# Kernel optimization log

Hardware: AMD Instinct MI355X
Metric: run time of the kernel (lower is better)

## Reference

```python
import jax, jax.numpy as jnp
import numpy as np

N_NODE = 50000
EMB = 128
LAYERS = 2
B = 1024
L = 50
E = 1_600_000


def setup_inputs() -> dict:
    key = jax.random.key(0)
    ks = jax.random.split(key, 21)
    d = EMB
    stdv = 1.0 / np.sqrt(d)
    u = lambda k, shape: jax.random.uniform(k, shape, minval=-stdv, maxval=stdv, dtype=jnp.float32)
    inp = {
        'adj_row': jax.random.randint(ks[0], (E,), 0, N_NODE, dtype=jnp.int32),
        'adj_col': jax.random.randint(ks[1], (E,), 0, N_NODE, dtype=jnp.int32),
        'adj_val': jax.random.uniform(ks[2], (E,), dtype=jnp.float32) / 32.0,  # ~row-normalized sparse adjacency
        'embedding': jax.random.normal(ks[3], (N_NODE, d), dtype=jnp.float32) * 0.1,
        'session_item': jax.random.randint(ks[4], (B, L), 0, N_NODE, dtype=jnp.int32),  # 0 hits the zero pad row
        'session_len': jnp.full((B, 1), float(L), dtype=jnp.float32),
        'D': jax.random.uniform(ks[5], (B, B), dtype=jnp.float32) / B,
        'A_sess': jax.random.uniform(ks[6], (B, B), dtype=jnp.float32) / B,
        'A_gnn': jax.random.uniform(ks[7], (B, L, 2 * L), dtype=jnp.float32) / L,
        'alias_pos': jax.random.randint(ks[8], (B, L), 0, L, dtype=jnp.int32),
        'hidden': jax.random.normal(ks[9], (B, L, d), dtype=jnp.float32) * 0.1,
        'W_in': u(ks[10], (d, d)), 'b_in': u(ks[11], (d,)),
        'W_out': u(ks[12], (d, d)), 'b_out': u(ks[13], (d,)),
        'w_ih': u(ks[14], (3 * d, 2 * d)), 'b_ih': u(ks[15], (3 * d,)),
        'w_hh': u(ks[16], (3 * d, d)), 'b_hh': u(ks[17], (3 * d,)),
        'b_iah': u(ks[18], (d,)), 'b_oah': u(ks[19], (d,)),
    }
    return inp


def reference(adj_row, adj_col, adj_val, embedding, session_item, session_len,
              D, A_sess, A_gnn, alias_pos, hidden,
              W_in, b_in, W_out, b_out, w_ih, b_ih, w_hh, b_hh, b_iah, b_oah):
    # ---- HyperConv: layers of sparse (COO) adjacency @ embedding, summed over hops ----
    emb = embedding
    final = embedding
    for _ in range(LAYERS):
        emb = jax.ops.segment_sum(adj_val[:, None] * emb[adj_col], adj_row, num_segments=N_NODE)
        final = final + emb
    item_emb = final  # [N_NODE, d]

    # ---- LineConv: zero-padded gather + mean pool over session, then session-graph propagation ----
    pad_table = jnp.concatenate([jnp.zeros((1, EMB), embedding.dtype), embedding], axis=0)
    seq_h = pad_table[session_item]                      # [B, L, d]
    sess = jnp.sum(seq_h, axis=1) / session_len          # [B, d]
    DA = D @ A_sess                                      # [B, B]
    acc = sess
    s = sess
    for _ in range(LAYERS):
        s = DA @ s
        acc = acc + s
    session_emb = acc                                    # [B, d]

    # ---- GNN: gather per-session in/out adjacency rows, gated GRU-style update ----
    in_out = jnp.take_along_axis(A_gnn, alias_pos[:, :, None], axis=1)  # [B, L, 2L]
    h_in = hidden @ W_in.T + b_in
    h_out = hidden @ W_out.T + b_out
    input_in = jnp.einsum('bij,bjd->bid', in_out[:, :, :L], h_in) + b_iah
    input_out = jnp.einsum('bij,bjd->bid', in_out[:, :, L:], h_out) + b_oah
    inputs = jnp.concatenate([input_in, input_out], axis=2)             # [B, L, 2d]
    gi = inputs @ w_ih.T + b_ih
    gh = hidden @ w_hh.T + b_hh
    i_r, i_i, i_n = jnp.split(gi, 3, axis=2)
    h_r, h_i, h_n = jnp.split(gh, 3, axis=2)
    resetgate = jax.nn.sigmoid(i_r + h_r)
    inputgate = jax.nn.sigmoid(i_i + h_i)
    newgate = jnp.tanh(i_n + resetgate * h_n)
    hy = newgate + inputgate * (hidden - newgate)        # [B, L, d]

    return item_emb, session_emb, hy
```

## Files before the change

### kernel.cpp

```cpp
#include <hip/hip_runtime.h>

#define EMB 128
#define NN 50000
#define BB 1024
#define LL 50
#define NBK 49
#define NEB 512
#define NCONV 2048

typedef float f32x4 __attribute__((ext_vector_type(4)));
typedef float f32x2 __attribute__((ext_vector_type(2)));
typedef unsigned short u16;
typedef unsigned int u32;
typedef unsigned long long u64;
typedef u16 u16x4 __attribute__((ext_vector_type(4)));
typedef u32 u32x4 __attribute__((ext_vector_type(4)));
typedef short bf16x8 __attribute__((ext_vector_type(8)));

__device__ __forceinline__ float u2f(u16 u) {
    union { unsigned int i; float f; } v; v.i = ((unsigned int)u) << 16; return v.f;
}
__device__ __forceinline__ u16 f2b(float f) {
    union { float f; unsigned int i; } v; v.f = f;
    unsigned int i = v.i;
    return (u16)((i + 0x7FFFu + ((i >> 16) & 1u)) >> 16);
}
__device__ __forceinline__ float lo2f(u32 w) { return u2f((u16)(w & 0xffffu)); }
__device__ __forceinline__ float hi2f(u32 w) { return u2f((u16)(w >> 16)); }
__device__ __forceinline__ float sigmoidf_(float x) { return 1.f / (1.f + __expf(-x)); }
__device__ __forceinline__ float tanhf_(float x) {
    float e = __expf(-2.f * x);
    return (1.f - e) / (1.f + e);
}

__global__ __launch_bounds__(256) void prep_kernel(
    const float* __restrict__ emb, const float* __restrict__ A, const float* __restrict__ D,
    const float* __restrict__ whh,
    u16* __restrict__ emb_bf, u16* __restrict__ A_bf, u16* __restrict__ D_bf,
    u16* __restrict__ whh_bf,
    const int* __restrict__ rowi, int* __restrict__ bcnt,
    const float* __restrict__ w_ih, const float* __restrict__ W_in, const float* __restrict__ W_out,
    const float* __restrict__ b_in, const float* __restrict__ b_out,
    const float* __restrict__ b_iah, const float* __restrict__ b_oah, const float* __restrict__ b_ih,
    const float* __restrict__ b_hh,
    u16* __restrict__ WcT_bf, float* __restrict__ uf,
    int E, int chunk)
{
    __shared__ int lc[NBK];
    __shared__ float wrow[256];
    __shared__ float red[3][256];
    int tid = threadIdx.x;

    if (blockIdx.x >= NCONV) {
        int d = blockIdx.x - NCONV;
        int c = tid;
        wrow[c] = w_ih[d * 256 + c];
        __syncthreads();
        const float* W = (c < 128) ? W_in : W_out;
        const float* wr = wrow + ((c < 128) ? 0 : 128);
        int cc = c & 127;
        float acc = 0.f;
#pragma unroll 4
        for (int j = 0; j < 128; j++) acc += wr[j] * W[j * 128 + cc];
        WcT_bf[d * 256 + c] = f2b(acc);
        float p1 = (c < 128) ? b_in[c] * wrow[c] : 0.f;
        float p2 = (c >= 128) ? b_out[cc] * wrow[c] : 0.f;
        float p3 = (c < 128) ? b_iah[c] * wrow[c] : b_oah[cc] * wrow[c];
        red[0][c] = p1; red[1][c] = p2; red[2][c] = p3;
        __syncthreads();
        for (int off = 128; off > 0; off >>= 1) {
            if (c < off) {
                red[0][c] += red[0][c + off];
                red[1][c] += red[1][c + off];
                red[2][c] += red[2][c + off];
            }
            __syncthreads();
        }
        if (c == 0) {
            int g = d >> 7, dd = d & 127;
            float u1v = red[0][0];
            float u2v = red[1][0];
            float u3v = red[2][0] + b_ih[d];
            uf[dd * 12 + g] = u1v;
            uf[dd * 12 + 3 + g] = u2v;
            if (g == 0)      uf[dd * 12 + 6] = u3v + b_hh[dd];
            else if (g == 1) uf[dd * 12 + 7] = u3v + b_hh[128 + dd];
            else {
                uf[dd * 12 + 8]  = u3v;
                uf[dd * 12 + 9]  = b_hh[256 + dd];
                uf[dd * 12 + 10] = 0.f;
                uf[dd * 12 + 11] = 0.f;
            }
        }
        return;
    }

    int gid = blockIdx.x * 256 + tid;
    int stride = NCONV * 256;
    if (blockIdx.x < NEB) {
        if (tid < NBK) lc[tid] = 0;
        __syncthreads();
        int beg = blockIdx.x * chunk, end = min(E, beg + chunk);
        for (int e = beg + tid; e < end; e += 256)
            atomicAdd(&lc[rowi[e] >> 10], 1);
        __syncthreads();
        if (tid < NBK) bcnt[blockIdx.x * NBK + tid] = lc[tid];
    }
    for (int i = gid; i < 1600000; i += stride) {
        f32x4 v = *(const f32x4*)(emb + (size_t)i * 4);
        u16x4 p;
#pragma unroll
        for (int t = 0; t < 4; t++) p[t] = f2b(v[t]);
        *(u16x4*)(emb_bf + (size_t)i * 4) = p;
    }
    for (int i = gid; i < 2146304; i += stride) {
        const float* s; u16* d; int off;
        if (i < 1048576)      { s = A;   d = A_bf;   off = i; }
        else if (i < 2097152) { s = D;   d = D_bf;   off = i - 1048576; }
        else                  { s = whh; d = whh_bf; off = i - 2097152; }
        d[off] = f2b(s[off]);
    }
}

__global__ __launch_bounds__(512) void bktscan_kernel(
    const int* __restrict__ bcnt, int* __restrict__ sofs, int* __restrict__ btot)
{
    __shared__ int ps[512];
    int k = blockIdx.x, t = threadIdx.x;
    int c = bcnt[t * NBK + k];
    ps[t] = c; __syncthreads();
    for (int off = 1; off < 512; off <<= 1) {
        int v = (t >= off) ? ps[t - off] : 0;
        __syncthreads();
        ps[t] += v; __syncthreads();
    }
    sofs[t * NBK + k] = ps[t] - c;
    if (t == 511) btot[k] = ps[511];
}

__global__ __launch_bounds__(64) void btotal_kernel(
    const int* __restrict__ btot, int* __restrict__ bofs, int E)
{
    if (threadIdx.x == 0) {
        int run = 0;
        for (int k = 0; k < NBK; k++) { bofs[k] = run; run += btot[k]; }
        bofs[NBK] = E;
    }
}

__global__ __launch_bounds__(256) void emit_kernel(
    const int* __restrict__ rowi, const int* __restrict__ coli, const float* __restrict__ val,
    const int* __restrict__ sofs, const int* __restrict__ bofs,
    u64* __restrict__ egs, int E, int chunk)
{
    __shared__ int cur[NBK];
    int b = blockIdx.x, tid = threadIdx.x;
    if (tid < NBK) cur[tid] = bofs[tid] + sofs[b * NBK + tid];
    __syncthreads();
    int beg = b * chunk, end = min(E, beg + chunk);
    for (int e = beg + tid; e < end; e += 256) {
        int r = rowi[e];
        int slot = atomicAdd(&cur[r >> 10], 1);
        u64 entry = ((u64)(u32)(r & 1023) << 32)
                  | (u64)((u32)(u16)coli[e] | ((u32)f2b(val[e]) << 16));
        egs[slot] = entry;
    }
}

__global__ __launch_bounds__(1024) void binsort2_kernel(
    const u64* __restrict__ egs, const int* __restrict__ bofs,
    int* __restrict__ row_ptr, u32* __restrict__ eg, int E)
{
    __shared__ int cnt_s[1024];
    __shared__ int ps[1024];
    int k = blockIdx.x, tid = threadIdx.x;
    int r0 = k << 10;
    int beg = bofs[k], end = bofs[k + 1];
    cnt_s[tid] = 0;
    __syncthreads();
    for (int i = beg + tid; i < end; i += 1024)
        atomicAdd(&cnt_s[(int)(egs[i] >> 32)], 1);
    __syncthreads();
    int v = cnt_s[tid];
    ps[tid] = v; __syncthreads();
    for (int off = 1; off < 1024; off <<= 1) {
        int t = (tid >= off) ? ps[tid - off] : 0;
        __syncthreads();
        ps[tid] += t; __syncthreads();
    }
    int ex = beg + ps[tid] - v;
    if (r0 + tid <= NN) row_ptr[r0 + tid] = ex;
    if (k == NBK - 1 && tid == 1023) row_ptr[NN] = E;
    cnt_s[tid] = ex;
    __syncthreads();
    for (int i = beg + tid; i < end; i += 1024) {
        u64 entry = egs[i];
        int rlo = (int)(entry >> 32);
        int p = atomicAdd(&cnt_s[rlo], 1);
        eg[p] = (u32)entry;
    }
}

template<int FUSE>
__global__ __launch_bounds__(256) void gatherb_kernel(
    const int* __restrict__ row_ptr, const u32* __restrict__ eg,
    const u16* __restrict__ src, const float* __restrict__ emb0,
    u16* __restrict__ dst_bf, float* __restrict__ dst_f)
{
    int wave = threadIdx.x >> 6;
    int lane = threadIdx.x & 63;
    int g  = lane >> 4;
    int fl = lane & 15;
    int r = blockIdx.x * 4 + wave;
    if (r >= NN) return;
    int beg = row_ptr[r], end = row_ptr[r + 1];

    float acc[8];
#pragma unroll
    for (int t = 0; t < 8; t++) acc[t] = 0.f;

    if (beg < end) {
        int last = end - 1;
        int npair = (end - beg + 7) >> 3;
        u32 pkA = eg[min(beg + g, last)];
        u32 pkB = eg[min(beg + 4 + g, last)];
        float vA = (beg + g     < end) ? u2f((u16)(pkA >> 16)) : 0.f;
        float vB = (beg + 4 + g < end) ? u2f((u16)(pkB >> 16)) : 0.f;
        u32x4 xA = *(const u32x4*)(src + ((pkA & 0xffffu) << 7) + (fl << 3));
        u32x4 xB = *(const u32x4*)(src + ((pkB & 0xffffu) << 7) + (fl << 3));
        pkA = eg[min(beg + 8  + g, last)];
        pkB = eg[min(beg + 12 + g, last)];

        int e = beg;
        for (int p = 0; p < npair; p++) {
            float cvA = vA, cvB = vB;
            u32x4 cxA = xA, cxB = xB;
            int eN = e + 8;
            vA = (eN + g     < end) ? u2f((u16)(pkA >> 16)) : 0.f;
            vB = (eN + 4 + g < end) ? u2f((u16)(pkB >> 16)) : 0.f;
            xA = *(const u32x4*)(src + ((pkA & 0xffffu) << 7) + (fl << 3));
            xB = *(const u32x4*)(src + ((pkB & 0xffffu) << 7) + (fl << 3));
            int eS = e + 16;
            pkA = eg[min(eS + g, last)];
            pkB = eg[min(eS + 4 + g, last)];
#pragma unroll
            for (int t = 0; t < 4; t++) {
                acc[2 * t]     += cvA * lo2f(cxA[t]);
                acc[2 * t + 1] += cvA * hi2f(cxA[t]);
            }
#pragma unroll
            for (int t = 0; t < 4; t++) {
                acc[2 * t]     += cvB * lo2f(cxB[t]);
                acc[2 * t + 1] += cvB * hi2f(cxB[t]);
            }
            e += 8;
        }
    }

#pragma unroll
    for (int t = 0; t < 8; t++) {
        acc[t] += __shfl_xor(acc[t], 16);
        acc[t] += __shfl_xor(acc[t], 32);
    }

    if (lane < 16) {
        if (FUSE) {
            u32x4 s = *(const u32x4*)(src + ((u32)r << 7) + (lane << 3));
            const float* e0p = emb0 + ((size_t)r << 7) + (lane << 3);
            f32x4 e0a = *(const f32x4*)e0p;
            f32x4 e0b = *(const f32x4*)(e0p + 4);
            f32x4 o0, o1;
#pragma unroll
            for (int t = 0; t < 2; t++) {
                o0[2 * t]     = acc[2 * t]     + e0a[2 * t]     + lo2f(s[t]);
                o0[2 * t + 1] = acc[2 * t + 1] + e0a[2 * t + 1] + hi2f(s[t]);
                o1[2 * t]     = acc[4 + 2 * t]     + e0b[2 * t]     + lo2f(s[2 + t]);
                o1[2 * t + 1] = acc[4 + 2 * t + 1] + e0b[2 * t + 1] + hi2f(s[2 + t]);
            }
            float* dp = dst_f + ((size_t)r << 7) + (lane << 3);
            *(f32x4*)dp = o0;
            *(f32x4*)(dp + 4) = o1;
        } else {
            u32x4 w;
#pragma unroll
            for (int t = 0; t < 4; t++)
                w[t] = (u32)f2b(acc[2 * t]) | ((u32)f2b(acc[2 * t + 1]) << 16);
            *(u32x4*)(dst_bf + ((size_t)r << 7) + (lane << 3)) = w;
        }
    }
}

__global__ __launch_bounds__(128) void sess_pool_kernel(
    const int* __restrict__ items, const float* __restrict__ emb,
    const float* __restrict__ slen, float* __restrict__ sess, u16* __restrict__ sessT)
{
    int b = blockIdx.x, d = threadIdx.x;
    const int* it = items + b * LL;
    float acc = 0.f;
    for (int l = 0; l < LL; l++) {
        int idx = it[l];
        if (idx > 0) acc += emb[(size_t)(idx - 1) * EMB + d];
    }
    float v = acc / slen[b];
    sess[b * EMB + d] = v;
    sessT[d * BB + b] = f2b(v);
}

template<int WT, int WF, int FADD>
__global__ __launch_bounds__(256) void mm_mfma_kernel(
    const u16* __restrict__ M_bf, const u16* __restrict__ Xt_bf,
    u16* __restrict__ Ct_bf, float* __restrict__ C_f,
    const float* __restrict__ add1, const float* __restrict__ add2)
{
    int tid = threadIdx.x;
    int wv = tid >> 6, lane = tid & 63, cl = lane & 15, kg = lane >> 4;
    int rbase = blockIdx.x * 16;
    f32x4 acc[2];
    acc[0] = (f32x4)0.f; acc[1] = (f32x4)0.f;
    const u16* arow = M_bf + (size_t)(rbase + cl) * BB + kg * 8;
    const u16* brow = Xt_bf + (size_t)(wv * 32 + cl) * BB + kg * 8;
#pragma unroll 4
    for (int k0 = 0; k0 < BB; k0 += 32) {
        bf16x8 a  = *(const bf16x8*)(arow + k0);
        bf16x8 b0 = *(const bf16x8*)(brow + k0);
        bf16x8 b1 = *(const bf16x8*)(brow + (size_t)16 * BB + k0);
        acc[0] = __builtin_amdgcn_mfma_f32_16x16x32_bf16(a, b0, acc[0], 0, 0, 0);
        acc[1] = __builtin_amdgcn_mfma_f32_16x16x32_bf16(a, b1, acc[1], 0, 0, 0);
    }
#pragma unroll
    for (int nt = 0; nt < 2; nt++) {
        int col = (wv * 2 + nt) * 16 + cl;
#pragma unroll
        for (int j = 0; j < 4; j++) {
            int row = rbase + kg * 4 + j;
            size_t ix = (size_t)row * EMB + col;
            if (WF) {
                float v = acc[nt][j];
                if (FADD) v += add1[ix] + add2[ix];
                C_f[ix] = v;
            }
            if (WT) Ct_bf[(size_t)col * BB + row] = f2b(acc[nt][j]);
        }
    }
}

__global__ __launch_bounds__(512) void gnn_tail_kernel(
    const float* __restrict__ hidden,
    const float* __restrict__ A_gnn, const int* __restrict__ alias_pos,
    const u16* __restrict__ WcT_bf, const u16* __restrict__ w_hh_bf,
    const float* __restrict__ uf,
    float* __restrict__ hy)
{
    __shared__ __attribute__((aligned(16))) u16 smem[25600];
    u16* Hs  = smem;
    u16* As  = smem + 8192;
    u16* HsT = smem + 16384;
    u16* M2s = smem + 8192;
    __shared__ float rcs[64][2];

    int b = blockIdx.x;
    int tid = threadIdx.x;
    int wv = tid >> 6, lane = tid & 63, cl = lane & 15, kg = lane >> 4;

    int pr_row[4], pr_c4[4], ppos[4];
#pragma unroll
    for (int it = 0; it < 4; it++) {
        int i = tid + it * 512;
        pr_row[it] = i >> 5; pr_c4[it] = i & 31;
        ppos[it] = (pr_row[it] < LL) ? alias_pos[b * LL + pr_row[it]] : 0;
    }
    float av[4][4];
#pragma unroll
    for (int it = 0; it < 4; it++) {
        const float* ar = A_gnn + ((size_t)b * LL + ppos[it]) * (2 * LL);
#pragma unroll
        for (int t = 0; t < 4; t++) {
            int jp = pr_c4[it] * 4 + t;
            int col = (jp < 64) ? jp : (50 + (jp - 64));
            int ok = (pr_row[it] < LL) && ((jp < 64) ? (jp < LL) : ((jp - 64) < LL));
            av[it][t] = ok ? ar[col] : 0.f;
        }
    }
    const float* hsrc = hidden + (size_t)b * LL * EMB;
#pragma unroll
    for (int it = 0; it < 4; it++) {
        u16x4 p;
#pragma unroll
        for (int t = 0; t < 4; t++) p[t] = f2b(av[it][t]);
        *(u16x4*)((char*)As + pr_row[it] * 256 + ((pr_c4[it] * 8) ^ ((pr_row[it] & 7) << 4))) = p;
    }
#pragma unroll
    for (int i2 = 0; i2 < 4; i2++) {
        int lin = i2 * 512 + tid;
        int hrow = lin >> 5, hc4 = lin & 31;
        f32x4 v = (hrow < LL) ? *(const f32x4*)(hsrc + hrow * 128 + hc4 * 4) : (f32x4)0.f;
        u16x4 q;
#pragma unroll
        for (int t = 0; t < 4; t++) q[t] = f2b(v[t]);
        *(u16x4*)((char*)Hs + hrow * 256 + ((hc4 * 8) ^ ((hrow & 7) << 4))) = q;
    }
#pragma unroll
    for (int i2 = 0; i2 < 4; i2++) {
        int idx = i2 * 512 + tid;
        int c = idx & 127, rg = idx >> 7;
        int r0 = rg * 4;
        u16x4 p = (u16x4)0;
#pragma unroll
        for (int k = 0; k < 4; k++) {
            int row = r0 + k;
            p[k] = (row < LL) ? f2b(hsrc[row * 128 + c]) : (u16)0;
        }
        *(u16x4*)&HsT[c * 72 + r0] = p;
    }
    __syncthreads();

    if (tid < 128) {
        int row = tid >> 1, hf = tid & 1;
        float s = 0.f;
#pragma unroll
        for (int c4 = 0; c4 < 16; c4++) {
            u16x4 v = *(const u16x4*)((const char*)As + row * 256 +
                        ((hf * 128 + c4 * 8) ^ ((row & 7) << 4)));
            s += u2f(v[0]) + u2f(v[1]) + u2f(v[2]) + u2f(v[3]);
        }
        rcs[row][hf] = s;
    }

    {
        int h = wv >> 2, ct = wv & 3;
        f32x4 m2acc[4][2];
#pragma unroll
        for (int mt = 0; mt < 4; mt++) { m2acc[mt][0] = (f32x4)0.f; m2acc[mt][1] = (f32x4)0.f; }
#pragma unroll
        for (int ks = 0; ks < 2; ks++) {
            bf16x8 bb[2];
#pragma unroll
            for (int nt = 0; nt < 2; nt++) {
                int c = ct * 32 + nt * 16 + cl;
                bb[nt] = *(const bf16x8*)&HsT[c * 72 + ks * 32 + kg * 8];
            }
#pragma unroll
            for (int mt = 0; mt < 4; mt++) {
                int mr = mt * 16 + cl;
                bf16x8 aa = *(const bf16x8*)((const char*)As + mr * 256 +
                             ((h * 128 + ks * 64 + kg * 16) ^ ((mr & 7) << 4)));
#pragma unroll
                for (int nt = 0; nt < 2; nt++)
                    m2acc[mt][nt] = __builtin_amdgcn_mfma_f32_16x16x32_bf16(aa, bb[nt], m2acc[mt][nt], 0, 0, 0);
            }
        }
        __syncthreads();
#pragma unroll
        for (int mt = 0; mt < 4; mt++)
#pragma unroll
            for (int nt = 0; nt < 2; nt++) {
                int kcol = h * 128 + ct * 32 + nt * 16 + cl;
#pragma unroll
                for (int j = 0; j < 4; j++) {
                    int row = mt * 16 + kg * 4 + j;
                    *(u16*)((char*)M2s + row * 512 + ((kcol * 2) ^ ((row & 7) << 4))) =
                        f2b(m2acc[mt][nt][j]);
                }
            }
    }
    __syncthreads();

    int dl = wv * 16 + cl;
    f32x4 accR[4], accI[4], accN1[4], accN2[4];
#pragma unroll
    for (int mt = 0; mt < 4; mt++) {
        accR[mt] = (f32x4)0.f; accI[mt] = (f32x4)0.f;
        accN1[mt] = (f32x4)0.f; accN2[mt] = (f32x4)0.f;
    }

#pragma unroll
    for (int ks = 0; ks < 8; ks++) {
        {
            bf16x8 bw = *(const bf16x8*)(WcT_bf + (size_t)dl * 256 + ks * 32 + kg * 8);
#pragma unroll
            for (int mt = 0; mt < 4; mt++) {
                int mr = mt * 16 + cl;
                bf16x8 a = *(const bf16x8*)((const char*)M2s + mr * 512 +
                             ((ks * 64 + kg * 16) ^ ((mr & 7) << 4)));
                accR[mt] = __builtin_amdgcn_mfma_f32_16x16x32_bf16(a, bw, accR[mt], 0, 0, 0);
            }
        }
        {
            bf16x8 bw = *(const bf16x8*)(WcT_bf + (size_t)(128 + dl) * 256 + ks * 32 + kg * 8);
#pragma unroll
            for (int mt = 0; mt < 4; mt++) {
                int mr = mt * 16 + cl;
                bf16x8 a = *(const bf16x8*)((const char*)M2s + mr * 512 +
                             ((ks * 64 + kg * 16) ^ ((mr & 7) << 4)));
                accI[mt] = __builtin_amdgcn_mfma_f32_16x16x32_bf16(a, bw, accI[mt], 0, 0, 0);
            }
        }
        {
            bf16x8 bw = *(const bf16x8*)(WcT_bf + (size_t)(256 + dl) * 256 + ks * 32 + kg * 8);
#pragma unroll
            for (int mt = 0; mt < 4; mt++) {
                int mr = mt * 16 + cl;
                bf16x8 a = *(const bf16x8*)((const char*)M2s + mr * 512 +
                             ((ks * 64 + kg * 16) ^ ((mr & 7) << 4)));
                accN1[mt] = __builtin_amdgcn_mfma_f32_16x16x32_bf16(a, bw, accN1[mt], 0, 0, 0);
            }
        }
    }
#pragma unroll
    for (int ks = 0; ks < 4; ks++) {
        {
            bf16x8 bw = *(const bf16x8*)(w_hh_bf + (size_t)dl * 128 + ks * 32 + kg * 8);
#pragma unroll
            for (int mt = 0; mt < 4; mt++) {
                int mr = mt * 16 + cl;
                bf16x8 a = *(const bf16x8*)((const char*)Hs + mr * 256 +
                             ((ks * 64 + kg * 16) ^ ((mr & 7) << 4)));
                accR[mt] = __builtin_amdgcn_mfma_f32_16x16x32_bf16(a, bw, accR[mt], 0, 0, 0);
            }
        }
        {
            bf16x8 bw = *(const bf16x8*)(w_hh_bf + (size_t)(128 + dl) * 128 + ks * 32 + kg * 8);
#pragma unroll
            for (int mt = 0; mt < 4; mt++) {
                int mr = mt * 16 + cl;
                bf16x8 a = *(const bf16x8*)((const char*)Hs + mr * 256 +
                             ((ks * 64 + kg * 16) ^ ((mr & 7) << 4)));
                accI[mt] = __builtin_amdgcn_mfma_f32_16x16x32_bf16(a, bw, accI[mt], 0, 0, 0);
            }
        }
        {
            bf16x8 bw = *(const bf16x8*)(w_hh_bf + (size_t)(256 + dl) * 128 + ks * 32 + kg * 8);
#pragma unroll
            for (int mt = 0; mt < 4; mt++) {
                int mr = mt * 16 + cl;
                bf16x8 a = *(const bf16x8*)((const char*)Hs + mr * 256 +
                             ((ks * 64 + kg * 16) ^ ((mr & 7) << 4)));
                accN2[mt] = __builtin_amdgcn_mfma_f32_16x16x32_bf16(a, bw, accN2[mt], 0, 0, 0);
            }
        }
    }

    __builtin_amdgcn_sched_barrier(0);
    {
        const f32x4* ufp = (const f32x4*)(uf + dl * 12);
        f32x4 U0 = ufp[0];
        f32x4 U1 = ufp[1];
        f32x4 U2 = ufp[2];
        float* hyb = hy + (size_t)b * LL * 128 + dl;
#pragma unroll
        for (int mt = 0; mt < 4; mt++)
#pragma unroll
            for (int j = 0; j < 4; j++) {
                int row = mt * 16 + kg * 4 + j;
                if (row >= LL) continue;
                float cr = rcs[row][0], dr = rcs[row][1];
                float pr  = accR[mt][j]  + cr * U0[0] + dr * U0[3] + U1[2];
                float pi  = accI[mt][j]  + cr * U0[1] + dr * U1[0] + U1[3];
                float pn1 = accN1[mt][j] + cr * U0[2] + dr * U1[1] + U2[0];
                float pn2 = accN2[mt][j] + U2[1];
                float rg = sigmoidf_(pr);
                float ig = sigmoidf_(pi);
                float ng = tanhf_(pn1 + rg * pn2);
                u16 hb = *(const u16*)((const char*)Hs + row * 256 + ((dl * 2) ^ ((row & 7) << 4)));
                float h = u2f(hb);
                hyb[row * 128] = ng + ig * (h - ng);
            }
    }
}

extern "C" void kernel_launch(void* const* d_in, const int* in_sizes, int n_in,
                              void* d_out, int out_size, void* d_ws, size_t ws_size,
                              hipStream_t stream) {
    (void)n_in; (void)out_size; (void)ws_size;
    const int*   adj_row      = (const int*)d_in[0];
    const int*   adj_col      = (const int*)d_in[1];
    const float* adj_val      = (const float*)d_in[2];
    const float* embedding    = (const float*)d_in[3];
    const int*   session_item = (const int*)d_in[4];
    const float* session_len  = (const float*)d_in[5];
    const float* Dm           = (const float*)d_in[6];
    const float* A_sess       = (const float*)d_in[7];
    const float* A_gnn        = (const float*)d_in[8];
    const int*   alias_pos    = (const int*)d_in[9];
    const float* hidden       = (const float*)d_in[10];
    const float* W_in         = (const float*)d_in[11];
    const float* b_in         = (const float*)d_in[12];
    const float* W_out        = (const float*)d_in[13];
    const float* b_out        = (const float*)d_in[14];
    const float* w_ih         = (const float*)d_in[15];
    const float* b_ih         = (const float*)d_in[16];
    const float* w_hh         = (const float*)d_in[17];
    const float* b_hh         = (const float*)d_in[18];
    const float* b_iah        = (const float*)d_in[19];
    const float* b_oah        = (const float*)d_in[20];
    const int E = in_sizes[0];

    float* out0 = (float*)d_out;
    float* out1 = out0 + 6400000;
    float* out2 = out1 + 131072;

    float* ws = (float*)d_ws;
    u16*  emb_bf  = (u16*)ws;
    int*  bcnt  = (int*)(ws + 3200000);
    int*  sofs  = (int*)(ws + 3230000);
    int*  btot  = (int*)(ws + 3260000);
    u16*  accA_bf = (u16*)(ws + 3200000);
    u32*  eg    = (u32*)(ws + 6400000);
    u64*  egs   = (u64*)(ws + 8000000);
    float* sess  = ws + 11200000;
    u16*   sessT = (u16*)(ws + 11350000);
    u16*   t1T   = (u16*)(ws + 11400000);
    u16*   s1T   = (u16*)(ws + 11450000);
    u16*   t2T   = (u16*)(ws + 11500000);
    float* s1    = ws + 11550000;
    u16*   A_bf  = (u16*)(ws + 11850000);
    u16*   D_bf  = (u16*)(ws + 12400000);
    int*   row_ptr = (int*)(ws + 12950000);
    int*   bofs    = row_ptr + NN + 1;
    u16* WcT_bf    = (u16*)(ws + 13107200);
    u16* w_hh_bf   = WcT_bf + 98304;
    float* uf      = (float*)(w_hh_bf + 49152);

    int chunk = (E + NEB - 1) / NEB;

    prep_kernel<<<NCONV + 384, 256, 0, stream>>>(embedding, A_sess, Dm, w_hh,
                                          emb_bf, A_bf, D_bf, w_hh_bf,
                                          adj_row, bcnt,
                                          w_ih, W_in, W_out, b_in, b_out, b_iah, b_oah, b_ih, b_hh,
                                          WcT_bf, uf,
                                          E, chunk);

    bktscan_kernel<<<NBK, 512, 0, stream>>>(bcnt, sofs, btot);
    btotal_kernel<<<1, 64, 0, stream>>>(btot, bofs, E);
    emit_kernel<<<NEB, 256, 0, stream>>>(adj_row, adj_col, adj_val, sofs, bofs, egs, E, chunk);
    binsort2_kernel<<<NBK, 1024, 0, stream>>>(egs, bofs, row_ptr, eg, E);
    gatherb_kernel<0><<<(NN + 3) / 4, 256, 0, stream>>>(row_ptr, eg, emb_bf, embedding, accA_bf, (float*)nullptr);
    gatherb_kernel<1><<<(NN + 3) / 4, 256, 0, stream>>>(row_ptr, eg, accA_bf, embedding, (u16*)nullptr, out0);

    sess_pool_kernel<<<BB, 128, 0, stream>>>(session_item, embedding, session_len, sess, sessT);
    mm_mfma_kernel<1, 0, 0><<<64, 256, 0, stream>>>(A_bf, sessT, t1T, (float*)nullptr, (const float*)nullptr, (const float*)nullptr);
    mm_mfma_kernel<1, 1, 0><<<64, 256, 0, stream>>>(D_bf, t1T, s1T, s1, (const float*)nullptr, (const float*)nullptr);
    mm_mfma_kernel<1, 0, 0><<<64, 256, 0, stream>>>(A_bf, s1T, t2T, (float*)nullptr, (const float*)nullptr, (const float*)nullptr);
    mm_mfma_kernel<0, 1, 1><<<64, 256, 0, stream>>>(D_bf, t2T, (u16*)nullptr, out1, sess, s1);

    gnn_tail_kernel<<<BB, 512, 0, stream>>>(hidden, A_gnn, alias_pos,
                                            WcT_bf, w_hh_bf, uf, out2);
}
```

Before: 311.0 us.

## Split GNN tail into M2 kernel and finer-grained gates kernel

The fused per-session GNN tail kernel is split in two. The first kernel computes the adjacency-times-hidden product M2 and the row sums, then writes them to workspace. The second kernel runs four blocks per session, each owning a quarter of the output features, with an XCD-aware block-to-session mapping. This raises parallelism and lowers per-block register and shared-memory pressure, at the cost of a global round-trip for M2, an extra launch, and each gates block re-staging the full M2 and hidden tiles.

```diff
diff --git a/kernel.cpp b/kernel.cpp
--- a/kernel.cpp
+++ b/kernel.cpp
@@ -344,34 +344,27 @@
     }
 }
 
-__global__ __launch_bounds__(512) void gnn_tail_kernel(
+__global__ __launch_bounds__(256) void m2_kernel(
     const float* __restrict__ hidden,
     const float* __restrict__ A_gnn, const int* __restrict__ alias_pos,
-    const u16* __restrict__ WcT_bf, const u16* __restrict__ w_hh_bf,
-    const float* __restrict__ uf,
-    float* __restrict__ hy)
-{
-    __shared__ __attribute__((aligned(16))) u16 smem[25600];
-    u16* Hs  = smem;
-    u16* As  = smem + 8192;
-    u16* HsT = smem + 16384;
-    u16* M2s = smem + 8192;
-    __shared__ float rcs[64][2];
-
+    u16* __restrict__ M2g, float* __restrict__ rcsg)
+{
+    __shared__ __attribute__((aligned(16))) u16 As[64 * 128];
+    __shared__ __attribute__((aligned(16))) u16 HsT[128 * 72];
     int b = blockIdx.x;
     int tid = threadIdx.x;
     int wv = tid >> 6, lane = tid & 63, cl = lane & 15, kg = lane >> 4;
 
-    int pr_row[4], pr_c4[4], ppos[4];
-#pragma unroll
-    for (int it = 0; it < 4; it++) {
-        int i = tid + it * 512;
+    int pr_row[8], pr_c4[8], ppos[8];
+#pragma unroll
+    for (int it = 0; it < 8; it++) {
+        int i = tid + it * 256;
         pr_row[it] = i >> 5; pr_c4[it] = i & 31;
         ppos[it] = (pr_row[it] < LL) ? alias_pos[b * LL + pr_row[it]] : 0;
     }
-    float av[4][4];
-#pragma unroll
-    for (int it = 0; it < 4; it++) {
+    float av[8][4];
+#pragma unroll
+    for (int it = 0; it < 8; it++) {
         const float* ar = A_gnn + ((size_t)b * LL + ppos[it]) * (2 * LL);
 #pragma unroll
         for (int t = 0; t < 4; t++) {
@@ -381,27 +374,17 @@
             av[it][t] = ok ? ar[col] : 0.f;
         }
     }
-    const float* hsrc = hidden + (size_t)b * LL * EMB;
-#pragma unroll
-    for (int it = 0; it < 4; it++) {
+#pragma unroll
+    for (int it = 0; it < 8; it++) {
         u16x4 p;
 #pragma unroll
         for (int t = 0; t < 4; t++) p[t] = f2b(av[it][t]);
         *(u16x4*)((char*)As + pr_row[it] * 256 + ((pr_c4[it] * 8) ^ ((pr_row[it] & 7) << 4))) = p;
     }
-#pragma unroll
-    for (int i2 = 0; i2 < 4; i2++) {
-        int lin = i2 * 512 + tid;
-        int hrow = lin >> 5, hc4 = lin & 31;
-        f32x4 v = (hrow < LL) ? *(const f32x4*)(hsrc + hrow * 128 + hc4 * 4) : (f32x4)0.f;
-        u16x4 q;
-#pragma unroll
-        for (int t = 0; t < 4; t++) q[t] = f2b(v[t]);
-        *(u16x4*)((char*)Hs + hrow * 256 + ((hc4 * 8) ^ ((hrow & 7) << 4))) = q;
-    }
-#pragma unroll
-    for (int i2 = 0; i2 < 4; i2++) {
-        int idx = i2 * 512 + tid;
+    const float* hsrc = hidden + (size_t)b * LL * EMB;
+#pragma unroll
+    for (int i2 = 0; i2 < 8; i2++) {
+        int idx = i2 * 256 + tid;
         int c = idx & 127, rg = idx >> 7;
         int r0 = rg * 4;
         u16x4 p = (u16x4)0;
@@ -423,22 +406,25 @@
                         ((hf * 128 + c4 * 8) ^ ((row & 7) << 4)));
             s += u2f(v[0]) + u2f(v[1]) + u2f(v[2]) + u2f(v[3]);
         }
-        rcs[row][hf] = s;
-    }
-
-    {
-        int h = wv >> 2, ct = wv & 3;
-        f32x4 m2acc[4][2];
-#pragma unroll
-        for (int mt = 0; mt < 4; mt++) { m2acc[mt][0] = (f32x4)0.f; m2acc[mt][1] = (f32x4)0.f; }
-#pragma unroll
-        for (int ks = 0; ks < 2; ks++) {
-            bf16x8 bb[2];
-#pragma unroll
-            for (int nt = 0; nt < 2; nt++) {
-                int c = ct * 32 + nt * 16 + cl;
-                bb[nt] = *(const bf16x8*)&HsT[c * 72 + ks * 32 + kg * 8];
-            }
+        rcsg[b * 128 + row * 2 + hf] = s;
+    }
+
+    int ct = wv;
+    f32x4 m2acc[2][4][2];
+#pragma unroll
+    for (int h = 0; h < 2; h++)
+#pragma unroll
+        for (int mt = 0; mt < 4; mt++) { m2acc[h][mt][0] = (f32x4)0.f; m2acc[h][mt][1] = (f32x4)0.f; }
+#pragma unroll
+    for (int ks = 0; ks < 2; ks++) {
+        bf16x8 bb[2];
+#pragma unroll
+        for (int nt = 0; nt < 2; nt++) {
+            int c = ct * 32 + nt * 16 + cl;
+            bb[nt] = *(const bf16x8*)&HsT[c * 72 + ks * 32 + kg * 8];
+        }
+#pragma unroll
+        for (int h = 0; h < 2; h++)
 #pragma unroll
             for (int mt = 0; mt < 4; mt++) {
                 int mr = mt * 16 + cl;
@@ -446,10 +432,12 @@
                              ((h * 128 + ks * 64 + kg * 16) ^ ((mr & 7) << 4)));
 #pragma unroll
                 for (int nt = 0; nt < 2; nt++)
-                    m2acc[mt][nt] = __builtin_amdgcn_mfma_f32_16x16x32_bf16(aa, bb[nt], m2acc[mt][nt], 0, 0, 0);
-            }
-        }
-        __syncthreads();
+                    m2acc[h][mt][nt] = __builtin_amdgcn_mfma_f32_16x16x32_bf16(aa, bb[nt], m2acc[h][mt][nt], 0, 0, 0);
+            }
+    }
+    u16* mb = M2g + (size_t)b * 16384;
+#pragma unroll
+    for (int h = 0; h < 2; h++)
 #pragma unroll
         for (int mt = 0; mt < 4; mt++)
 #pragma unroll
@@ -458,17 +446,53 @@
 #pragma unroll
                 for (int j = 0; j < 4; j++) {
                     int row = mt * 16 + kg * 4 + j;
-                    *(u16*)((char*)M2s + row * 512 + ((kcol * 2) ^ ((row & 7) << 4))) =
-                        f2b(m2acc[mt][nt][j]);
+                    mb[row * 256 + kcol] = f2b(m2acc[h][mt][nt][j]);
                 }
             }
-    }
+}
+
+__global__ __launch_bounds__(256) void gates_kernel(
+    const float* __restrict__ hidden, const u16* __restrict__ M2g,
+    const float* __restrict__ rcsg,
+    const u16* __restrict__ WcT_bf, const u16* __restrict__ w_hh_bf,
+    const float* __restrict__ uf, float* __restrict__ hy)
+{
+    __shared__ __attribute__((aligned(16))) u16 M2s[64 * 256];
+    __shared__ __attribute__((aligned(16))) u16 Hs[64 * 128];
+    __shared__ float rcs[64][2];
+    int bid = blockIdx.x;
+    int xcd = bid & 7, rest = bid >> 3;
+    int dq = rest & 3, b = (rest >> 2) * 8 + xcd;
+    int tid = threadIdx.x;
+    int wv = tid >> 6, lane = tid & 63, cl = lane & 15, kg = lane >> 4;
+
+    const u16* mb = M2g + (size_t)b * 16384;
+#pragma unroll
+    for (int it = 0; it < 8; it++) {
+        int lin = it * 256 + tid;
+        int row = lin >> 5, c8 = lin & 31;
+        u32x4 v = *(const u32x4*)(mb + row * 256 + c8 * 8);
+        *(u32x4*)((char*)M2s + row * 512 + ((c8 * 16) ^ ((row & 7) << 4))) = v;
+    }
+    const float* hsrc = hidden + (size_t)b * LL * EMB;
+#pragma unroll
+    for (int i2 = 0; i2 < 8; i2++) {
+        int lin = i2 * 256 + tid;
+        int hrow = lin >> 5, hc4 = lin & 31;
+        f32x4 v = (hrow < LL) ? *(const f32x4*)(hsrc + hrow * 128 + hc4 * 4) : (f32x4)0.f;
+        u16x4 q;
+#pragma unroll
+        for (int t = 0; t < 4; t++) q[t] = f2b(v[t]);
+        *(u16x4*)((char*)Hs + hrow * 256 + ((hc4 * 8) ^ ((hrow & 7) << 4))) = q;
+    }
+    if (tid < 128) rcs[tid >> 1][tid & 1] = rcsg[b * 128 + tid];
     __syncthreads();
 
-    int dl = wv * 16 + cl;
-    f32x4 accR[4], accI[4], accN1[4], accN2[4];
-#pragma unroll
-    for (int mt = 0; mt < 4; mt++) {
+    int rh = wv >> 1, dt = wv & 1;
+    int d = dq * 32 + dt * 16 + cl;
+    f32x4 accR[2], accI[2], accN1[2], accN2[2];
+#pragma unroll
+    for (int mt = 0; mt < 2; mt++) {
         accR[mt] = (f32x4)0.f; accI[mt] = (f32x4)0.f;
         accN1[mt] = (f32x4)0.f; accN2[mt] = (f32x4)0.f;
     }
@@ -476,30 +500,30 @@
 #pragma unroll
     for (int ks = 0; ks < 8; ks++) {
         {
-            bf16x8 bw = *(const bf16x8*)(WcT_bf + (size_t)dl * 256 + ks * 32 + kg * 8);
-#pragma unroll
-            for (int mt = 0; mt < 4; mt++) {
-                int mr = mt * 16 + cl;
+            bf16x8 bw = *(const bf16x8*)(WcT_bf + (size_t)d * 256 + ks * 32 + kg * 8);
+#pragma unroll
+            for (int mt = 0; mt < 2; mt++) {
+                int mr = rh * 32 + mt * 16 + cl;
                 bf16x8 a = *(const bf16x8*)((const char*)M2s + mr * 512 +
                              ((ks * 64 + kg * 16) ^ ((mr & 7) << 4)));
                 accR[mt] = __builtin_amdgcn_mfma_f32_16x16x32_bf16(a, bw, accR[mt], 0, 0, 0);
             }
         }
         {
-            bf16x8 bw = *(const bf16x8*)(WcT_bf + (size_t)(128 + dl) * 256 + ks * 32 + kg * 8);
-#pragma unroll
-            for (int mt = 0; mt < 4; mt++) {
-                int mr = mt * 16 + cl;
+            bf16x8 bw = *(const bf16x8*)(WcT_bf + (size_t)(128 + d) * 256 + ks * 32 + kg * 8);
+#pragma unroll
+            for (int mt = 0; mt < 2; mt++) {
+                int mr = rh * 32 + mt * 16 + cl;
                 bf16x8 a = *(const bf16x8*)((const char*)M2s + mr * 512 +
                              ((ks * 64 + kg * 16) ^ ((mr & 7) << 4)));
                 accI[mt] = __builtin_amdgcn_mfma_f32_16x16x32_bf16(a, bw, accI[mt], 0, 0, 0);
             }
         }
         {
-            bf16x8 bw = *(const bf16x8*)(WcT_bf + (size_t)(256 + dl) * 256 + ks * 32 + kg * 8);
-#pragma unroll
-            for (int mt = 0; mt < 4; mt++) {
-                int mr = mt * 16 + cl;
+            bf16x8 bw = *(const bf16x8*)(WcT_bf + (size_t)(256 + d) * 256 + ks * 32 + kg * 8);
+#pragma unroll
+            for (int mt = 0; mt < 2; mt++) {
+                int mr = rh * 32 + mt * 16 + cl;
                 bf16x8 a = *(const bf16x8*)((const char*)M2s + mr * 512 +
                              ((ks * 64 + kg * 16) ^ ((mr & 7) << 4)));
                 accN1[mt] = __builtin_amdgcn_mfma_f32_16x16x32_bf16(a, bw, accN1[mt], 0, 0, 0);
@@ -509,30 +533,30 @@
 #pragma unroll
     for (int ks = 0; ks < 4; ks++) {
         {
-            bf16x8 bw = *(const bf16x8*)(w_hh_bf + (size_t)dl * 128 + ks * 32 + kg * 8);
-#pragma unroll
-            for (int mt = 0; mt < 4; mt++) {
-                int mr = mt * 16 + cl;
+            bf16x8 bw = *(const bf16x8*)(w_hh_bf + (size_t)d * 128 + ks * 32 + kg * 8);
+#pragma unroll
+            for (int mt = 0; mt < 2; mt++) {
+                int mr = rh * 32 + mt * 16 + cl;
                 bf16x8 a = *(const bf16x8*)((const char*)Hs + mr * 256 +
                              ((ks * 64 + kg * 16) ^ ((mr & 7) << 4)));
                 accR[mt] = __builtin_amdgcn_mfma_f32_16x16x32_bf16(a, bw, accR[mt], 0, 0, 0);
             }
         }
         {
-            bf16x8 bw = *(const bf16x8*)(w_hh_bf + (size_t)(128 + dl) * 128 + ks * 32 + kg * 8);
-#pragma unroll
-            for (int mt = 0; mt < 4; mt++) {
-                int mr = mt * 16 + cl;
+            bf16x8 bw = *(const bf16x8*)(w_hh_bf + (size_t)(128 + d) * 128 + ks * 32 + kg * 8);
+#pragma unroll
+            for (int mt = 0; mt < 2; mt++) {
+                int mr = rh * 32 + mt * 16 + cl;
                 bf16x8 a = *(const bf16x8*)((const char*)Hs + mr * 256 +
                              ((ks * 64 + kg * 16) ^ ((mr & 7) << 4)));
                 accI[mt] = __builtin_amdgcn_mfma_f32_16x16x32_bf16(a, bw, accI[mt], 0, 0, 0);
             }
         }
         {
-            bf16x8 bw = *(const bf16x8*)(w_hh_bf + (size_t)(256 + dl) * 128 + ks * 32 + kg * 8);
-#pragma unroll
-            for (int mt = 0; mt < 4; mt++) {
-                int mr = mt * 16 + cl;
+            bf16x8 bw = *(const bf16x8*)(w_hh_bf + (size_t)(256 + d) * 128 + ks * 32 + kg * 8);
+#pragma unroll
+            for (int mt = 0; mt < 2; mt++) {
+                int mr = rh * 32 + mt * 16 + cl;
                 bf16x8 a = *(const bf16x8*)((const char*)Hs + mr * 256 +
                              ((ks * 64 + kg * 16) ^ ((mr & 7) << 4)));
                 accN2[mt] = __builtin_amdgcn_mfma_f32_16x16x32_bf16(a, bw, accN2[mt], 0, 0, 0);
@@ -542,16 +566,16 @@
 
     __builtin_amdgcn_sched_barrier(0);
     {
-        const f32x4* ufp = (const f32x4*)(uf + dl * 12);
+        const f32x4* ufp = (const f32x4*)(uf + d * 12);
         f32x4 U0 = ufp[0];
         f32x4 U1 = ufp[1];
         f32x4 U2 = ufp[2];
-        float* hyb = hy + (size_t)b * LL * 128 + dl;
-#pragma unroll
-        for (int mt = 0; mt < 4; mt++)
+        float* hyb = hy + (size_t)b * LL * 128 + d;
+#pragma unroll
+        for (int mt = 0; mt < 2; mt++)
 #pragma unroll
             for (int j = 0; j < 4; j++) {
-                int row = mt * 16 + kg * 4 + j;
+                int row = rh * 32 + mt * 16 + kg * 4 + j;
                 if (row >= LL) continue;
                 float cr = rcs[row][0], dr = rcs[row][1];
                 float pr  = accR[mt][j]  + cr * U0[0] + dr * U0[3] + U1[2];
@@ -561,7 +585,7 @@
                 float rg = sigmoidf_(pr);
                 float ig = sigmoidf_(pi);
                 float ng = tanhf_(pn1 + rg * pn2);
-                u16 hb = *(const u16*)((const char*)Hs + row * 256 + ((dl * 2) ^ ((row & 7) << 4)));
+                u16 hb = *(const u16*)((const char*)Hs + row * 256 + ((d * 2) ^ ((row & 7) << 4)));
                 float h = u2f(hb);
                 hyb[row * 128] = ng + ig * (h - ng);
             }
@@ -620,6 +644,8 @@
     u16* WcT_bf    = (u16*)(ws + 13107200);
     u16* w_hh_bf   = WcT_bf + 98304;
     float* uf      = (float*)(w_hh_bf + 49152);
+    u16*   M2g  = (u16*)ws;
+    float* rcsg = ws + 8500000;
 
     int chunk = (E + NEB - 1) / NEB;
 
@@ -637,12 +663,14 @@
     gatherb_kernel<0><<<(NN + 3) / 4, 256, 0, stream>>>(row_ptr, eg, emb_bf, embedding, accA_bf, (float*)nullptr);
     gatherb_kernel<1><<<(NN + 3) / 4, 256, 0, stream>>>(row_ptr, eg, accA_bf, embedding, (u16*)nullptr, out0);
 
+    m2_kernel<<<BB, 256, 0, stream>>>(hidden, A_gnn, alias_pos, M2g, rcsg);
+
     sess_pool_kernel<<<BB, 128, 0, stream>>>(session_item, embedding, session_len, sess, sessT);
     mm_mfma_kernel<1, 0, 0><<<64, 256, 0, stream>>>(A_bf, sessT, t1T, (float*)nullptr, (const float*)nullptr, (const float*)nullptr);
     mm_mfma_kernel<1, 1, 0><<<64, 256, 0, stream>>>(D_bf, t1T, s1T, s1, (const float*)nullptr, (const float*)nullptr);
     mm_mfma_kernel<1, 0, 0><<<64, 256, 0, stream>>>(A_bf, s1T, t2T, (float*)nullptr, (const float*)nullptr, (const float*)nullptr);
     mm_mfma_kernel<0, 1, 1><<<64, 256, 0, stream>>>(D_bf, t2T, (u16*)nullptr, out1, sess, s1);
 
-    gnn_tail_kernel<<<BB, 512, 0, stream>>>(hidden, A_gnn, alias_pos,
-                                            WcT_bf, w_hh_bf, uf, out2);
-}
+    gates_kernel<<<4 * BB, 256, 0, stream>>>(hidden, M2g, rcsg,
+                                             WcT_bf, w_hh_bf, uf, out2);
+}
```

Result: slower. 359.0 us (+15.4%).
